# Kernel tuning notes

Hardware: AMD Instinct MI355X
Metric: run time of the kernel (lower is better)

## Reference

```python
import jax, jax.numpy as jnp
import numpy as np

EPS = 1e-9

def setup_inputs() -> dict:
    key = jax.random.key(0)
    k1, k2 = jax.random.split(key)
    B, N, D = 8, 48, 2
    gt_points = jax.random.normal(k1, (B, N, D), dtype=jnp.float32)
    cos_similarity = jax.random.uniform(k2, (B, N, N), dtype=jnp.float32)
    threshold = jnp.array([0.5], dtype=jnp.float32)
    return {"gt_points": gt_points, "cos_similarity": cos_similarity, "threshold": threshold}

def reference(gt_points, cos_similarity, threshold):
    B, N, D = gt_points.shape
    # zero out low-similarity pairs (torch in-place masked assign -> pure where)
    sm = jnp.where(cos_similarity < threshold, jnp.float32(0), cos_similarity)
    # pairwise difference vectors scaled by similarity: [B, N, N, D] -> [B, N*N, D]
    vectors = (gt_points[:, :, None, :] - gt_points[:, None, :, :]) * sm[..., None]
    vectors = vectors.reshape(B, N * N, D)
    # all-pairs dot products: batched GEMM instead of broadcasting to [B,M,M,D]
    dot = jnp.einsum('bmd,bnd->bmn', vectors, vectors)  # [B, M, M]
    idx_num = jnp.sum(dot != 0).astype(dot.dtype)
    dot = jnp.abs(dot)
    # per-vector norm with torch's per-element eps: sqrt(sum(v*v + 1e-9, axis=D))
    vabs = jnp.sqrt(jnp.sum(vectors * vectors + EPS, axis=2))  # [B, M]
    abs_dot = vabs[:, :, None] * vabs[:, None, :]  # [B, M, M]
    abs_dot = jnp.where(abs_dot == 0, jnp.float32(1), abs_dot)
    return jnp.sum(dot / abs_dot) / idx_num
```

## Files before the change

### kernel.cpp

```cpp
#include <hip/hip_runtime.h>
#include <stdint.h>

#define B_     8
#define N_     48
#define M_     (N_ * N_)
#define RPB    16
#define CHUNKS (M_ / RPB)
#define NBLK   (B_ * CHUNKS)
#define TPB    256

__global__ __launch_bounds__(TPB) void pair_kernel(
    const float* __restrict__ gt,
    const float* __restrict__ sm,
    const float* __restrict__ thrp,
    float* __restrict__ partS,
    unsigned int* __restrict__ partC)
{
    __shared__ float4 tile[M_];
    __shared__ float  gx[N_], gy[N_];
    __shared__ float  redS[4];
    __shared__ unsigned int redC[4];

    const int tid   = threadIdx.x;
    const int b     = blockIdx.x / CHUNKS;
    const int chunk = blockIdx.x % CHUNKS;

    if (tid < N_) {
        float2 g = ((const float2*)gt)[b * N_ + tid];
        gx[tid] = g.x;
        gy[tid] = g.y;
    }
    __syncthreads();

    const float thr = thrp[0];
    for (int idx = tid; idx < M_; idx += TPB) {
        float s = sm[b * M_ + idx];
        s = (s < thr) ? 0.0f : s;
        int i = idx / N_;
        int j = idx - i * N_;
        float vx = __fmul_rn(__fsub_rn(gx[i], gx[j]), s);
        float vy = __fmul_rn(__fsub_rn(gy[i], gy[j]), s);
        float ss = vx * vx + vy * vy + 2e-9f;
        tile[idx] = make_float4(vx, vy, rsqrtf(ss), 0.0f);
    }
    __syncthreads();

    const int m0 = chunk * RPB;
    float total = 0.0f;
    unsigned int cnt = 0;

    #pragma unroll
    for (int g = 0; g < RPB / 4; ++g) {
        const float4 r0 = tile[m0 + g * 4 + 0];
        const float4 r1 = tile[m0 + g * 4 + 1];
        const float4 r2 = tile[m0 + g * 4 + 2];
        const float4 r3 = tile[m0 + g * 4 + 3];
        float a0 = 0.0f, a1 = 0.0f, a2 = 0.0f, a3 = 0.0f;
        for (int n = tid; n < M_; n += TPB) {
            const float4 c = tile[n];
            float d0 = __fadd_rn(__fmul_rn(r0.x, c.x), __fmul_rn(r0.y, c.y));
            float d1 = __fadd_rn(__fmul_rn(r1.x, c.x), __fmul_rn(r1.y, c.y));
            float d2 = __fadd_rn(__fmul_rn(r2.x, c.x), __fmul_rn(r2.y, c.y));
            float d3 = __fadd_rn(__fmul_rn(r3.x, c.x), __fmul_rn(r3.y, c.y));
            cnt += (d0 != 0.0f);
            cnt += (d1 != 0.0f);
            cnt += (d2 != 0.0f);
            cnt += (d3 != 0.0f);
            a0 = fmaf(fabsf(d0), c.z, a0);
            a1 = fmaf(fabsf(d1), c.z, a1);
            a2 = fmaf(fabsf(d2), c.z, a2);
            a3 = fmaf(fabsf(d3), c.z, a3);
        }
        total = fmaf(a0, r0.z, total);
        total = fmaf(a1, r1.z, total);
        total = fmaf(a2, r2.z, total);
        total = fmaf(a3, r3.z, total);
    }

    for (int off = 32; off > 0; off >>= 1) {
        total += __shfl_down(total, off, 64);
        cnt   += __shfl_down(cnt,   off, 64);
    }
    const int wave = tid >> 6;
    if ((tid & 63) == 0) { redS[wave] = total; redC[wave] = cnt; }
    __syncthreads();
    if (tid == 0) {
        partS[blockIdx.x] = redS[0] + redS[1] + redS[2] + redS[3];
        partC[blockIdx.x] = redC[0] + redC[1] + redC[2] + redC[3];
    }
}

__global__ __launch_bounds__(256) void finalize_kernel(
    const float* __restrict__ partS,
    const unsigned int* __restrict__ partC,
    float* __restrict__ out)
{
    __shared__ double rs[4];
    __shared__ double rc[4];
    const int tid = threadIdx.x;
    double s = 0.0, c = 0.0;
    for (int i = tid; i < NBLK; i += 256) {
        s += (double)partS[i];
        c += (double)partC[i];
    }
    for (int off = 32; off > 0; off >>= 1) {
        s += __shfl_down(s, off, 64);
        c += __shfl_down(c, off, 64);
    }
    const int wave = tid >> 6;
    if ((tid & 63) == 0) { rs[wave] = s; rc[wave] = c; }
    __syncthreads();
    if (tid == 0) {
        double stot = rs[0] + rs[1] + rs[2] + rs[3];
        double ctot = rc[0] + rc[1] + rc[2] + rc[3];
        out[0] = (float)(stot / ctot);
    }
}

extern "C" void kernel_launch(void* const* d_in, const int* in_sizes, int n_in,
                              void* d_out, int out_size, void* d_ws, size_t ws_size,
                              hipStream_t stream) {
    const float* gt  = (const float*)d_in[0];
    const float* sm  = (const float*)d_in[1];
    const float* thr = (const float*)d_in[2];

    float*        partS = (float*)d_ws;
    unsigned int* partC = (unsigned int*)((char*)d_ws + NBLK * sizeof(float));

    pair_kernel<<<NBLK, TPB, 0, stream>>>(gt, sm, thr, partS, partC);
    finalize_kernel<<<1, 256, 0, stream>>>(partS, partC, (float*)d_out);
}
```

Before: 73.95 us.

## Register-tile 18 rows per thread and fuse finalize via last-block ticket

Each block now handles 18 rows held in registers, and one loop over columns reuses every shared-memory column load across all 18 rows. There are also fewer blocks, so the per-block rebuild of the shared tile is repeated less often. The separate finalize kernel is replaced by an atomic ticket, and the last block to finish does the final reduction; a memset resets the ticket. This raises register pressure and adds a threadfence/atomic per block.

Result: slower. 98.90 us (+33.7%).

```diff
diff --git a/kernel.cpp b/kernel.cpp
--- a/kernel.cpp
+++ b/kernel.cpp
@@ -1,29 +1,36 @@
 #include <hip/hip_runtime.h>
 #include <stdint.h>
 
-#define B_     8
-#define N_     48
-#define M_     (N_ * N_)
-#define RPB    16
-#define CHUNKS (M_ / RPB)
-#define NBLK   (B_ * CHUNKS)
-#define TPB    256
+#define B_      8
+#define N_      48
+#define M_      (N_ * N_)
+#define ROWS    18
+#define CPB     (M_ / ROWS)
+#define NBLK    (B_ * CPB)
+#define TPB     256
 
-__global__ __launch_bounds__(TPB) void pair_kernel(
+#define WS_PARTS_OFF   0
+#define WS_PARTC_OFF   (NBLK * sizeof(float))
+#define WS_TICKET_OFF  (2 * NBLK * sizeof(float))
+
+__global__ __launch_bounds__(TPB, 4) void fused_kernel(
     const float* __restrict__ gt,
     const float* __restrict__ sm,
     const float* __restrict__ thrp,
     float* __restrict__ partS,
-    unsigned int* __restrict__ partC)
+    unsigned int* __restrict__ partC,
+    unsigned int* __restrict__ ticket,
+    float* __restrict__ out)
 {
     __shared__ float4 tile[M_];
     __shared__ float  gx[N_], gy[N_];
     __shared__ float  redS[4];
     __shared__ unsigned int redC[4];
+    __shared__ int amLast;
 
     const int tid   = threadIdx.x;
-    const int b     = blockIdx.x / CHUNKS;
-    const int chunk = blockIdx.x % CHUNKS;
+    const int b     = blockIdx.x >> 7;
+    const int chunk = blockIdx.x & (CPB - 1);
 
     if (tid < N_) {
         float2 g = ((const float2*)gt)[b * N_ + tid];
@@ -45,37 +52,29 @@
     }
     __syncthreads();
 
-    const int m0 = chunk * RPB;
+    const int m0 = chunk * ROWS;
+    float rx[ROWS], ry[ROWS], rw[ROWS], acc[ROWS];
+    #pragma unroll
+    for (int r = 0; r < ROWS; ++r) {
+        float4 t = tile[m0 + r];
+        rx[r] = t.x; ry[r] = t.y; rw[r] = t.z; acc[r] = 0.0f;
+    }
+
+    unsigned int cnt = 0;
+    for (int n = tid; n < M_; n += TPB) {
+        const float4 c = tile[n];
+        #pragma unroll
+        for (int r = 0; r < ROWS; ++r) {
+            float d = __fadd_rn(__fmul_rn(rx[r], c.x), __fmul_rn(ry[r], c.y));
+            cnt += (d != 0.0f) ? 1u : 0u;
+            acc[r] = fmaf(fabsf(d), c.z, acc[r]);
+        }
+    }
+
     float total = 0.0f;
-    unsigned int cnt = 0;
-
     #pragma unroll
-    for (int g = 0; g < RPB / 4; ++g) {
-        const float4 r0 = tile[m0 + g * 4 + 0];
-        const float4 r1 = tile[m0 + g * 4 + 1];
-        const float4 r2 = tile[m0 + g * 4 + 2];
-        const float4 r3 = tile[m0 + g * 4 + 3];
-        float a0 = 0.0f, a1 = 0.0f, a2 = 0.0f, a3 = 0.0f;
-        for (int n = tid; n < M_; n += TPB) {
-            const float4 c = tile[n];
-            float d0 = __fadd_rn(__fmul_rn(r0.x, c.x), __fmul_rn(r0.y, c.y));
-            float d1 = __fadd_rn(__fmul_rn(r1.x, c.x), __fmul_rn(r1.y, c.y));
-            float d2 = __fadd_rn(__fmul_rn(r2.x, c.x), __fmul_rn(r2.y, c.y));
-            float d3 = __fadd_rn(__fmul_rn(r3.x, c.x), __fmul_rn(r3.y, c.y));
-            cnt += (d0 != 0.0f);
-            cnt += (d1 != 0.0f);
-            cnt += (d2 != 0.0f);
-            cnt += (d3 != 0.0f);
-            a0 = fmaf(fabsf(d0), c.z, a0);
-            a1 = fmaf(fabsf(d1), c.z, a1);
-            a2 = fmaf(fabsf(d2), c.z, a2);
-            a3 = fmaf(fabsf(d3), c.z, a3);
-        }
-        total = fmaf(a0, r0.z, total);
-        total = fmaf(a1, r1.z, total);
-        total = fmaf(a2, r2.z, total);
-        total = fmaf(a3, r3.z, total);
-    }
+    for (int r = 0; r < ROWS; ++r)
+        total = fmaf(acc[r], rw[r], total);
 
     for (int off = 32; off > 0; off >>= 1) {
         total += __shfl_down(total, off, 64);
@@ -87,33 +86,29 @@
     if (tid == 0) {
         partS[blockIdx.x] = redS[0] + redS[1] + redS[2] + redS[3];
         partC[blockIdx.x] = redC[0] + redC[1] + redC[2] + redC[3];
+        __threadfence();
+        unsigned int t = atomicAdd(ticket, 1u);
+        amLast = (t == NBLK - 1) ? 1 : 0;
     }
-}
+    __syncthreads();
 
-__global__ __launch_bounds__(256) void finalize_kernel(
-    const float* __restrict__ partS,
-    const unsigned int* __restrict__ partC,
-    float* __restrict__ out)
-{
-    __shared__ double rs[4];
-    __shared__ double rc[4];
-    const int tid = threadIdx.x;
-    double s = 0.0, c = 0.0;
-    for (int i = tid; i < NBLK; i += 256) {
-        s += (double)partS[i];
-        c += (double)partC[i];
-    }
-    for (int off = 32; off > 0; off >>= 1) {
-        s += __shfl_down(s, off, 64);
-        c += __shfl_down(c, off, 64);
-    }
-    const int wave = tid >> 6;
-    if ((tid & 63) == 0) { rs[wave] = s; rc[wave] = c; }
-    __syncthreads();
-    if (tid == 0) {
-        double stot = rs[0] + rs[1] + rs[2] + rs[3];
-        double ctot = rc[0] + rc[1] + rc[2] + rc[3];
-        out[0] = (float)(stot / ctot);
+    if (amLast) {
+        __threadfence();
+        __shared__ double rs[4], rc[4];
+        double s = 0.0, c = 0.0;
+        for (int i = tid; i < NBLK; i += TPB) {
+            s += (double)partS[i];
+            c += (double)partC[i];
+        }
+        for (int off = 32; off > 0; off >>= 1) {
+            s += __shfl_down(s, off, 64);
+            c += __shfl_down(c, off, 64);
+        }
+        if ((tid & 63) == 0) { rs[wave] = s; rc[wave] = c; }
+        __syncthreads();
+        if (tid == 0)
+            out[0] = (float)((rs[0] + rs[1] + rs[2] + rs[3]) /
+                             (rc[0] + rc[1] + rc[2] + rc[3]));
     }
 }
 
@@ -124,9 +119,11 @@
     const float* sm  = (const float*)d_in[1];
     const float* thr = (const float*)d_in[2];
 
-    float*        partS = (float*)d_ws;
-    unsigned int* partC = (unsigned int*)((char*)d_ws + NBLK * sizeof(float));
+    float*        partS  = (float*)((char*)d_ws + WS_PARTS_OFF);
+    unsigned int* partC  = (unsigned int*)((char*)d_ws + WS_PARTC_OFF);
+    unsigned int* ticket = (unsigned int*)((char*)d_ws + WS_TICKET_OFF);
 
-    pair_kernel<<<NBLK, TPB, 0, stream>>>(gt, sm, thr, partS, partC);
-    finalize_kernel<<<1, 256, 0, stream>>>(partS, partC, (float*)d_out);
+    hipMemsetAsync(ticket, 0, sizeof(unsigned int), stream);
+    fused_kernel<<<NBLK, TPB, 0, stream>>>(gt, sm, thr, partS, partC, ticket,
+                                           (float*)d_out);
 }
```
